# Performance work log

Measured on AMD Instinct MI355X. Metric: run time of the kernel, lower is better.

Reference implementation:

```python
import jax, jax.numpy as jnp
import numpy as np

N_HEAD, D_MODEL, D_HEAD = 16, 1024, 64
QLEN, BSZ, RLEN = 2048, 2, 2048
SCALE = 1.0 / (D_HEAD ** 0.5)


def setup_inputs() -> dict:
    key = jax.random.key(0)
    ks = jax.random.split(key, 7)
    return {
        "w": jax.random.normal(ks[0], (QLEN, BSZ, D_MODEL), dtype=jnp.float32),
        "r": jax.random.normal(ks[1], (RLEN, D_MODEL), dtype=jnp.float32),
        "qkv_w": jax.random.normal(ks[2], (D_MODEL, 3 * N_HEAD * D_HEAD), dtype=jnp.float32) * 0.02,
        "r_net_w": jax.random.normal(ks[3], (D_MODEL, N_HEAD * D_HEAD), dtype=jnp.float32) * 0.02,
        "o_w": jax.random.normal(ks[4], (N_HEAD * D_HEAD, D_MODEL), dtype=jnp.float32) * 0.02,
        "r_r_bias": jax.random.normal(ks[5], (N_HEAD, D_HEAD), dtype=jnp.float32) * 0.02,
        "r_w_bias": jax.random.normal(ks[6], (N_HEAD, D_HEAD), dtype=jnp.float32) * 0.02,
    }


def _rel_shift(x):
    # x: [qlen, rlen, bsz, n_head]
    q, r, b, n = x.shape
    x = jnp.pad(x, ((0, 0), (1, 0), (0, 0), (0, 0)))
    x = x.reshape(r + 1, q, b, n)[1:]
    return x.reshape(q, r, b, n)


def reference(w, r, qkv_w, r_net_w, o_w, r_r_bias, r_w_bias):
    qlen, bsz, _ = w.shape
    rlen = r.shape[0]
    # qkv projection: [qlen, bsz, 3*H*D]
    w_heads = jnp.einsum('ibm,mh->ibh', w, qkv_w)
    w_head_q, w_head_k, w_head_v = jnp.split(w_heads, 3, axis=-1)
    klen = w_head_k.shape[0]
    w_head_q = w_head_q.reshape(qlen, bsz, N_HEAD, D_HEAD)
    w_head_k = w_head_k.reshape(klen, bsz, N_HEAD, D_HEAD)
    w_head_v = w_head_v.reshape(klen, bsz, N_HEAD, D_HEAD)
    # relative position keys: [rlen, H, D]
    r_head_k = jnp.einsum('jm,mh->jh', r, r_net_w).reshape(rlen, N_HEAD, D_HEAD)

    rw_head_q = w_head_q + r_w_bias  # content bias
    rr_head_q = w_head_q + r_r_bias  # position bias
    AC = jnp.einsum('ibnd,jbnd->ijbn', rw_head_q, w_head_k)
    BD = jnp.einsum('ibnd,jnd->ijbn', rr_head_q, r_head_k)
    BD = _rel_shift(BD)[:, :klen]

    attn_score = (AC + BD) * SCALE
    attn_prob = jax.nn.softmax(attn_score, axis=1)  # over klen axis
    attn_vec = jnp.einsum('ijbn,jbnd->ibnd', attn_prob, w_head_v)
    attn_vec = attn_vec.reshape(qlen, bsz, N_HEAD * D_HEAD)
    attn_out = jnp.einsum('ibh,hm->ibm', attn_vec, o_w)
    return (w + attn_out, attn_prob, AC, BD)
```

## Files before the change

### kernel.cpp

```cpp
#include <hip/hip_runtime.h>
#include <hip/hip_bf16.h>


typedef unsigned short u16;
typedef __attribute__((ext_vector_type(8))) short short8;
typedef __attribute__((ext_vector_type(4))) float f32x4;
typedef __attribute__((ext_vector_type(4))) unsigned short u16x4;

__device__ __forceinline__ u16 f2bf(float x){
  unsigned u = __float_as_uint(x);
  u += 0x7fffu + ((u >> 16) & 1u);
  return (u16)(u >> 16);
}
__device__ __forceinline__ float bf2f(u16 s){
  return __uint_as_float(((unsigned)s) << 16);
}
__device__ __forceinline__ f32x4 mfma16(short8 a, short8 b, f32x4 c){
  return __builtin_amdgcn_mfma_f32_16x16x32_bf16(a, b, c, 0, 0, 0);
}
__device__ __forceinline__ void ntst4(float* p, f32x4 v){
  __builtin_nontemporal_store(v, (f32x4*)p);
}


__global__ __launch_bounds__(256) void k_cast(const float* __restrict__ src, u16* __restrict__ dst, int n4){
  int i = blockIdx.x * 256 + threadIdx.x;
  if (i >= n4) return;
  f32x4 v = *(const f32x4*)(src + (size_t)i * 4);
  u16x4 o;
  #pragma unroll
  for (int q = 0; q < 4; ++q) o[q] = f2bf(v[q]);
  *(u16x4*)(dst + (size_t)i * 4) = o;
}

__global__ __launch_bounds__(256) void k_tc(const float* __restrict__ src, u16* __restrict__ dst, int R, int C){
  __shared__ float ld[32][33];
  int c0 = blockIdx.x * 32, r0 = blockIdx.y * 32;
  int t = threadIdx.x;
  int r = t >> 3, c4 = (t & 7) * 4;
  f32x4 v = *(const f32x4*)(src + (size_t)(r0 + r) * C + c0 + c4);
  #pragma unroll
  for (int q = 0; q < 4; ++q) ld[r][c4 + q] = v[q];
  __syncthreads();
  int c = t >> 3, r4 = (t & 7) * 4;
  u16x4 o;
  #pragma unroll
  for (int q = 0; q < 4; ++q) o[q] = f2bf(ld[r4 + q][c]);
  *(u16x4*)(dst + (size_t)(c0 + c) * R + r0 + r4) = o;
}


template<int MODE>
__global__ __launch_bounds__(512) void k_gemm(const u16* __restrict__ A, const u16* __restrict__ Bt,
        u16* __restrict__ o0, u16* __restrict__ o1, u16* __restrict__ o2,
        const float* __restrict__ wres, float* __restrict__ outf)
{
  __shared__ __align__(16) u16 As[128][40];
  __shared__ __align__(16) u16 Bs[256][40];
  const int t = threadIdx.x;
  const int wave = t >> 6, lane = t & 63;
  const int wr = wave >> 2, wc = wave & 3;
  const int g = lane >> 4, li = lane & 15;
  const int m0 = blockIdx.x * 128, n0 = blockIdx.y * 256;
  f32x4 acc[4][4] = {};
  const int ar = t >> 2, ac8 = (t & 3) * 8;
  for (int kt = 0; kt < 32; ++kt){
    int k0 = kt * 32;
    *(short8*)&As[ar][ac8] = *(const short8*)(A + (size_t)(m0 + ar) * 1024 + k0 + ac8);
    #pragma unroll
    for (int u = 0; u < 2; ++u){
      int id = t + 512 * u; int br = id >> 2, bc8 = (id & 3) * 8;
      *(short8*)&Bs[br][bc8] = *(const short8*)(Bt + (size_t)(n0 + br) * 1024 + k0 + bc8);
    }
    __syncthreads();
    short8 af[4], bfv[4];
    #pragma unroll
    for (int mf = 0; mf < 4; ++mf) af[mf] = *(const short8*)&As[wr * 64 + mf * 16 + li][g * 8];
    #pragma unroll
    for (int nf = 0; nf < 4; ++nf) bfv[nf] = *(const short8*)&Bs[wc * 64 + nf * 16 + li][g * 8];
    #pragma unroll
    for (int mf = 0; mf < 4; ++mf)
      #pragma unroll
      for (int nf = 0; nf < 4; ++nf)
        acc[mf][nf] = mfma16(af[mf], bfv[nf], acc[mf][nf]);
    __syncthreads();
  }
  #pragma unroll
  for (int mf = 0; mf < 4; ++mf)
  #pragma unroll
  for (int nf = 0; nf < 4; ++nf)
  #pragma unroll
  for (int r = 0; r < 4; ++r){
    int gr = m0 + wr * 64 + mf * 16 + g * 4 + r;
    int gc = n0 + wc * 64 + nf * 16 + li;
    float v = acc[mf][nf][r];
    if (MODE == 0){
      int part = gc >> 10, hh = gc & 1023;
      int hn = hh >> 6, d = hh & 63;
      int i = gr >> 1, b = gr & 1;
      u16* dst = (part == 0) ? o0 : ((part == 1) ? o1 : o2);
      dst[((((b << 4) + hn) * 2048 + i) << 6) + d] = f2bf(v);
    } else if (MODE == 1){
      int hn = gc >> 6, d = gc & 63;
      o0[((hn * 2048 + gr) << 6) + d] = f2bf(v);
    } else {
      size_t idx = (size_t)gr * 1024 + gc;
      outf[idx] = wres[idx] + v;
    }
  }
}

__global__ __launch_bounds__(256) void k_bias(const u16* __restrict__ Km, const float* __restrict__ bv,
                                              float* __restrict__ out, int total){
  int idx = blockIdx.x * 256 + threadIdx.x;
  if (idx >= total) return;
  int n = (idx >> 11) & 15;
  const u16* kr = Km + ((size_t)idx << 6);
  const float* bp = bv + n * 64;
  float s = 0.f;
  #pragma unroll
  for (int d8 = 0; d8 < 8; ++d8){
    short8 v = *(const short8*)(kr + d8 * 8);
    #pragma unroll
    for (int q = 0; q < 8; ++q) s += bp[d8 * 8 + q] * bf2f((u16)v[q]);
  }
  out[idx] = s;
}

__global__ __launch_bounds__(256) void k_trv(const u16* __restrict__ V, u16* __restrict__ Vt){
  __shared__ __align__(16) u16 ld[64][72];
  int bn = blockIdx.x, j0 = blockIdx.y * 64;
  int t = threadIdx.x;
  #pragma unroll
  for (int u = 0; u < 2; ++u){
    int id = t + 256 * u; int r = id >> 3, c8 = (id & 7) * 8;
    *(short8*)&ld[r][c8] = *(const short8*)(V + ((size_t)(bn * 2048 + j0 + r) << 6) + c8);
  }
  __syncthreads();
  #pragma unroll
  for (int u = 0; u < 2; ++u){
    int id = t + 256 * u; int d = id >> 3, j8 = (id & 7) * 8;
    short8 o;
    #pragma unroll
    for (int q = 0; q < 8; ++q) o[q] = ld[j8 + q][d];
    *(short8*)(Vt + ((size_t)(bn * 64 + d) << 11) + j0 + j8) = o;
  }
}

__global__ __launch_bounds__(512, 4) void k_statsR(const u16* __restrict__ Q, const u16* __restrict__ RK,
        const u16* __restrict__ Kc, const float* __restrict__ bias_ac, const float* __restrict__ bias_bd,
        float* __restrict__ ACo, float* __restrict__ BDo,
        float* __restrict__ m_part, float* __restrict__ l_part)
{
  __shared__ u16 sBD[2][16 * 544];
  __shared__ u16 sB[32 * 271];
  const int t = threadIdx.x, wave = t >> 6, lane = t & 63;
  const int g = lane >> 4, li = lane & 15;
  const int i0 = blockIdx.x * 16, b = blockIdx.y;
  const int jbase = blockIdx.z * 512;
  short8 qa[2][2], qb[2][2];
  #pragma unroll
  for (int nn = 0; nn < 2; ++nn){
    int bn = b * 16 + wave * 2 + nn;
    const u16* qp = Q + ((size_t)(bn * 2048 + i0 + li) << 6) + g * 8;
    qa[nn][0] = *(const short8*)qp;
    qa[nn][1] = *(const short8*)(qp + 32);
    int rowB = i0 + 1 + li; if (rowB > 2047) rowB = 2047;
    const u16* qp2 = Q + ((size_t)(bn * 2048 + rowB) << 6) + g * 8;
    qb[nn][0] = *(const short8*)qp2;
    qb[nn][1] = *(const short8*)(qp2 + 32);
  }
  for (int w2 = t; w2 < 2 * 4352; w2 += 512) ((unsigned*)sBD)[w2] = 0;

  float m_[2][4], l_[2][4];
  #pragma unroll
  for (int nn = 0; nn < 2; ++nn)
    #pragma unroll
    for (int r = 0; r < 4; ++r){ m_[nn][r] = -__builtin_inff(); l_[nn][r] = 0.f; }

  int cur = 0;
  for (int ch = 0; ch < 16; ++ch){
    int j0 = jbase + ch * 32;
    int m = j0 - i0;
    __syncthreads();
    u16* bufA = &sBD[cur][0];
    u16* bufB = &sBD[cur ^ 1][0];

    auto do_tile = [&](int c0, bool case2){
      if (c0 < 0 || c0 > 2032) return;
      int off = c0 - m + (case2 ? 2 : -2047);
      #pragma unroll
      for (int nn = 0; nn < 2; ++nn){
        int n = wave * 2 + nn;
        const u16* rp = RK + ((size_t)(n * 2048 + c0 + li) << 6) + g * 8;
        short8 b0 = *(const short8*)rp;
        short8 b1 = *(const short8*)(rp + 32);
        f32x4 acc = {};
        acc = mfma16(case2 ? qb[nn][0] : qa[nn][0], b0, acc);
        acc = mfma16(case2 ? qb[nn][1] : qa[nn][1], b1, acc);
        float bb = bias_bd[n * 2048 + c0 + li];
        #pragma unroll
        for (int r = 0; r < 4; ++r){
          int fr = g * 4 + r;
          int jw = li + fr + off;
          u16 val = f2bf(acc[r] + bb);
          if ((unsigned)jw < 32u)       bufA[fr * 544 + jw * 17 + n] = val;
          else if ((unsigned)jw < 64u)  bufB[fr * 544 + (jw - 32) * 17 + n] = val;
        }
      }
    };
    if (ch == 0){
      do_tile(m + 2032, false);
      do_tile(m - 32, true);
      do_tile(m - 16, true);
    }
    do_tile(m + 2048, false);
    do_tile(m + 2064, false);
    do_tile(m, true);
    do_tile(m + 16, true);
    __syncthreads();

    #pragma unroll
    for (int nn = 0; nn < 2; ++nn){
      int n = wave * 2 + nn, bn = b * 16 + n;
      float sv[2][4];
      #pragma unroll
      for (int cf = 0; cf < 2; ++cf){
        int jc = j0 + cf * 16 + li;
        const u16* kp = Kc + ((size_t)(bn * 2048 + jc) << 6) + g * 8;
        short8 b0 = *(const short8*)kp;
        short8 b1 = *(const short8*)(kp + 32);
        f32x4 acc = {};
        acc = mfma16(qa[nn][0], b0, acc);
        acc = mfma16(qa[nn][1], b1, acc);
        float ba = bias_ac[bn * 2048 + jc];
        #pragma unroll
        for (int r = 0; r < 4; ++r){
          float av = acc[r] + ba;
          sB[(cf * 16 + li) * 271 + n * 17 + g * 4 + r] = f2bf(av);
          float bd = bf2f(bufA[(g * 4 + r) * 544 + (cf * 16 + li) * 17 + n]);
          sv[cf][r] = (av + bd) * 0.125f;
        }
      }
      float cm[4], mn[4], ps[4];
      #pragma unroll
      for (int r = 0; r < 4; ++r) cm[r] = fmaxf(sv[0][r], sv[1][r]);
      #pragma unroll
      for (int off = 1; off < 16; off <<= 1)
        #pragma unroll
        for (int r = 0; r < 4; ++r) cm[r] = fmaxf(cm[r], __shfl_xor(cm[r], off));
      #pragma unroll
      for (int r = 0; r < 4; ++r){
        mn[r] = fmaxf(m_[nn][r], cm[r]);
        ps[r] = __expf(sv[0][r] - mn[r]) + __expf(sv[1][r] - mn[r]);
      }
      #pragma unroll
      for (int off = 1; off < 16; off <<= 1)
        #pragma unroll
        for (int r = 0; r < 4; ++r) ps[r] += __shfl_xor(ps[r], off);
      #pragma unroll
      for (int r = 0; r < 4; ++r){
        l_[nn][r] = l_[nn][r] * __expf(m_[nn][r] - mn[r]) + ps[r];
        m_[nn][r] = mn[r];
      }
    }
    #pragma unroll
    for (int u = 0; u < 4; ++u){
      int flat4 = t + 512 * u;
      int n4 = (flat4 & 3) * 4, jl = (flat4 >> 2) & 31, row = flat4 >> 7;
      f32x4 v;
      #pragma unroll
      for (int q = 0; q < 4; ++q) v[q] = bf2f(bufA[row * 544 + jl * 17 + n4 + q]);
      ntst4(BDo + (((size_t)(i0 + row) * 2048 + j0 + jl) << 5) + b * 16 + n4, v);
    }
    __syncthreads();
    #pragma unroll
    for (int u = 0; u < 4; ++u){
      int flat4 = t + 512 * u;
      int n4 = (flat4 & 3) * 4, jl = (flat4 >> 2) & 31, row = flat4 >> 7;
      f32x4 v;
      #pragma unroll
      for (int q = 0; q < 4; ++q) v[q] = bf2f(sB[jl * 271 + (n4 + q) * 17 + row]);
      ntst4(ACo + (((size_t)(i0 + row) * 2048 + j0 + jl) << 5) + b * 16 + n4, v);
    }
    for (int w2 = t; w2 < 4352; w2 += 512) ((unsigned*)bufA)[w2] = 0;
    cur ^= 1;
  }
  if (li == 0){
    #pragma unroll
    for (int nn = 0; nn < 2; ++nn)
      #pragma unroll
      for (int r = 0; r < 4; ++r){
        int bn = b * 16 + wave * 2 + nn;
        size_t o = ((size_t)(blockIdx.z * 32 + bn)) * 2048 + i0 + g * 4 + r;
        m_part[o] = m_[nn][r];
        l_part[o] = l_[nn][r];
      }
  }
}

__global__ __launch_bounds__(256) void k_comb(const float* __restrict__ mp, const float* __restrict__ lp,
                                              float* __restrict__ mf, float* __restrict__ lf){
  int idx = blockIdx.x * 256 + threadIdx.x;
  float m = -__builtin_inff();
  #pragma unroll
  for (int js = 0; js < 4; ++js) m = fmaxf(m, mp[js * 65536 + idx]);
  float l = 0.f;
  #pragma unroll
  for (int js = 0; js < 4; ++js) l += lp[js * 65536 + idx] * __expf(mp[js * 65536 + idx] - m);
  mf[idx] = m;
  lf[idx] = l;
}

__global__ __launch_bounds__(512, 4) void k_prob_pv(const u16* __restrict__ Q, const u16* __restrict__ Kc,
        const u16* __restrict__ Vt, const float* __restrict__ bias_ac, const float* __restrict__ BD,
        const float* __restrict__ m_f, const float* __restrict__ l_f,
        float* __restrict__ PROB, float* __restrict__ Ovp)
{
  __shared__ __align__(16) u16 sA[16 * 648];
  __shared__ u16 sB[32 * 271];
  const int t = threadIdx.x, wave = t >> 6, lane = t & 63;
  const int g = lane >> 4, li = lane & 15;
  const int i0 = blockIdx.x * 16, b = blockIdx.y;
  const int jbase = blockIdx.z * 512;
  short8 qa[2][2];
  float m_[2][4], rl_[2][4];
  #pragma unroll
  for (int nn = 0; nn < 2; ++nn){
    int bn = b * 16 + wave * 2 + nn;
    const u16* qp = Q + ((size_t)(bn * 2048 + i0 + li) << 6) + g * 8;
    qa[nn][0] = *(const short8*)qp;
    qa[nn][1] = *(const short8*)(qp + 32);
    #pragma unroll
    for (int r = 0; r < 4; ++r){
      m_[nn][r]  = m_f[bn * 2048 + i0 + g * 4 + r];
      rl_[nn][r] = 1.f / l_f[bn * 2048 + i0 + g * 4 + r];
    }
  }
  f32x4 oacc[2][4] = {};

  f32x4 pfv[4];
  #pragma unroll
  for (int u = 0; u < 4; ++u){
    int flat4 = t + 512 * u;
    int n4 = (flat4 & 3) * 4, jl = (flat4 >> 2) & 31, row = flat4 >> 7;
    pfv[u] = *(const f32x4*)(BD + (((size_t)(i0 + row) * 2048 + jbase + jl) << 5) + b * 16 + n4);
  }

  for (int ch = 0; ch < 16; ++ch){
    int j0 = jbase + ch * 32;
    __syncthreads();
    #pragma unroll
    for (int u = 0; u < 4; ++u){
      int flat4 = t + 512 * u;
      int n4 = (flat4 & 3) * 4, jl = (flat4 >> 2) & 31, row = flat4 >> 7;
      u16x4 o;
      #pragma unroll
      for (int q = 0; q < 4; ++q) o[q] = (u16)(__float_as_uint(pfv[u][q]) >> 16);
      *(u16x4*)&sA[row * 648 + jl * 20 + n4] = o;
    }
    if (ch + 1 < 16){
      #pragma unroll
      for (int u = 0; u < 4; ++u){
        int flat4 = t + 512 * u;
        int n4 = (flat4 & 3) * 4, jl = (flat4 >> 2) & 31, row = flat4 >> 7;
        pfv[u] = *(const f32x4*)(BD + (((size_t)(i0 + row) * 2048 + j0 + 32 + jl) << 5) + b * 16 + n4);
      }
    }
    __syncthreads();
    #pragma unroll
    for (int nn = 0; nn < 2; ++nn){
      int n = wave * 2 + nn, bn = b * 16 + n;
      #pragma unroll
      for (int cf = 0; cf < 2; ++cf){
        int jc = j0 + cf * 16 + li;
        const u16* kp = Kc + ((size_t)(bn * 2048 + jc) << 6) + g * 8;
        short8 b0 = *(const short8*)kp;
        short8 b1 = *(const short8*)(kp + 32);
        f32x4 acc = {};
        acc = mfma16(qa[nn][0], b0, acc);
        acc = mfma16(qa[nn][1], b1, acc);
        float ba = bias_ac[bn * 2048 + jc];
        #pragma unroll
        for (int r = 0; r < 4; ++r){
          float bd = bf2f(sA[(g * 4 + r) * 648 + (cf * 16 + li) * 20 + n]);
          float s = (acc[r] + ba + bd) * 0.125f;
          float p = __expf(s - m_[nn][r]) * rl_[nn][r];
          sB[(cf * 16 + li) * 271 + n * 17 + g * 4 + r] = f2bf(p);
        }
      }
    }
    #pragma unroll
    for (int nn = 0; nn < 2; ++nn){
      int n = wave * 2 + nn, bn = b * 16 + n;
      short8 pa;
      #pragma unroll
      for (int tt = 0; tt < 8; ++tt) pa[tt] = (short)sB[(g * 8 + tt) * 271 + n * 17 + li];
      const u16* vb = Vt + ((size_t)(bn * 64) << 11) + j0 + g * 8;
      #pragma unroll
      for (int vf = 0; vf < 4; ++vf){
        short8 bv = *(const short8*)(vb + ((size_t)(vf * 16 + li) << 11));
        oacc[nn][vf] = mfma16(pa, bv, oacc[nn][vf]);
      }
    }
    __syncthreads();
    #pragma unroll
    for (int u = 0; u < 4; ++u){
      int flat4 = t + 512 * u;
      int n4 = (flat4 & 3) * 4, jl = (flat4 >> 2) & 31, row = flat4 >> 7;
      f32x4 v;
      #pragma unroll
      for (int q = 0; q < 4; ++q) v[q] = bf2f(sB[jl * 271 + (n4 + q) * 17 + row]);
      ntst4(PROB + (((size_t)(i0 + row) * 2048 + j0 + jl) << 5) + b * 16 + n4, v);
    }
  }
  float* op = Ovp + (size_t)blockIdx.z * 4194304;
  #pragma unroll
  for (int nn = 0; nn < 2; ++nn){
    int n = wave * 2 + nn;
    #pragma unroll
    for (int vf = 0; vf < 4; ++vf)
      #pragma unroll
      for (int r = 0; r < 4; ++r)
        op[(size_t)((i0 + g * 4 + r) * 2 + b) * 1024 + n * 64 + vf * 16 + li] = oacc[nn][vf][r];
  }
}

__global__ __launch_bounds__(256) void k_ovred(const float* __restrict__ ovp, u16* __restrict__ ov){
  int i = blockIdx.x * 256 + threadIdx.x;
  const f32x4* p = (const f32x4*)ovp;
  f32x4 s = p[i];
  #pragma unroll
  for (int js = 1; js < 4; ++js) s += p[(size_t)js * 1048576 + i];
  u16x4 o;
  #pragma unroll
  for (int q = 0; q < 4; ++q) o[q] = f2bf(s[q]);
  ((u16x4*)ov)[i] = o;
}


extern "C" void kernel_launch(void* const* d_in, const int* in_sizes, int n_in,
                              void* d_out, int out_size, void* d_ws, size_t ws_size,
                              hipStream_t stream)
{
  const float* w      = (const float*)d_in[0];
  const float* r      = (const float*)d_in[1];
  const float* qkv_w  = (const float*)d_in[2];
  const float* rnet_w = (const float*)d_in[3];
  const float* o_w    = (const float*)d_in[4];
  const float* rrb    = (const float*)d_in[5];
  const float* rwb    = (const float*)d_in[6];

  char* ws = (char*)d_ws;
  size_t off = 0;
  auto alloc = [&](size_t bytes) -> void* {
    void* p = ws + off; off += (bytes + 255) & ~(size_t)255; return p;
  };
  u16* Xbf    = (u16*)alloc((size_t)4096 * 1024 * 2);
  u16* Rbf    = (u16*)alloc((size_t)2048 * 1024 * 2);
  u16* Wqkvt  = (u16*)alloc((size_t)3072 * 1024 * 2);
  u16* Wrt    = (u16*)alloc((size_t)1024 * 1024 * 2);
  u16* Wot    = (u16*)alloc((size_t)1024 * 1024 * 2);
  u16* Qs     = (u16*)alloc((size_t)32 * 2048 * 64 * 2);
  u16* Ks     = (u16*)alloc((size_t)32 * 2048 * 64 * 2);
  u16* Vs     = (u16*)alloc((size_t)32 * 2048 * 64 * 2);
  u16* Vts    = (u16*)alloc((size_t)32 * 64 * 2048 * 2);
  u16* RKs    = (u16*)alloc((size_t)16 * 2048 * 64 * 2);
  float* bias_ac = (float*)alloc((size_t)32 * 2048 * 4);
  float* bias_bd = (float*)alloc((size_t)16 * 2048 * 4);
  float* m_part  = (float*)alloc((size_t)4 * 32 * 2048 * 4);
  float* l_part  = (float*)alloc((size_t)4 * 32 * 2048 * 4);
  float* m_fin   = (float*)alloc((size_t)32 * 2048 * 4);
  float* l_fin   = (float*)alloc((size_t)32 * 2048 * 4);
  float* Ovp     = (float*)alloc((size_t)4 * 4096 * 1024 * 4);
  u16* Ov     = (u16*)alloc((size_t)4096 * 1024 * 2);

  float* out0 = (float*)d_out;
  float* PROB = out0 + 4194304;
  float* ACo  = PROB + 134217728;
  float* BDo  = ACo  + 134217728;

  k_cast<<<dim3(4096), dim3(256), 0, stream>>>(w, Xbf, 1048576);
  k_cast<<<dim3(2048), dim3(256), 0, stream>>>(r, Rbf, 524288);
  k_tc<<<dim3(96, 32), dim3(256), 0, stream>>>(qkv_w,  Wqkvt, 1024, 3072);
  k_tc<<<dim3(32, 32), dim3(256), 0, stream>>>(rnet_w, Wrt,   1024, 1024);
  k_tc<<<dim3(32, 32), dim3(256), 0, stream>>>(o_w,    Wot,   1024, 1024);
  k_gemm<0><<<dim3(32, 12), dim3(512), 0, stream>>>(Xbf, Wqkvt, Qs, Ks, Vs, nullptr, nullptr);
  k_gemm<1><<<dim3(16, 4),  dim3(512), 0, stream>>>(Rbf, Wrt,  RKs, nullptr, nullptr, nullptr, nullptr);
  k_bias<<<dim3(256), dim3(256), 0, stream>>>(Ks,  rwb, bias_ac, 65536);
  k_bias<<<dim3(128), dim3(256), 0, stream>>>(RKs, rrb, bias_bd, 32768);
  k_trv<<<dim3(32, 32), dim3(256), 0, stream>>>(Vs, Vts);
  k_statsR<<<dim3(128, 2, 4), dim3(512), 0, stream>>>(Qs, RKs, Ks, bias_ac, bias_bd, ACo, BDo, m_part, l_part);
  k_comb<<<dim3(256), dim3(256), 0, stream>>>(m_part, l_part, m_fin, l_fin);
  k_prob_pv<<<dim3(128, 2, 4), dim3(512), 0, stream>>>(Qs, Ks, Vts, bias_ac, BDo, m_fin, l_fin, PROB, Ovp);
  k_ovred<<<dim3(4096), dim3(256), 0, stream>>>(Ovp, Ov);
  k_gemm<2><<<dim3(32, 4), dim3(512), 0, stream>>>(Ov, Wot, nullptr, nullptr, nullptr, w, out0);
}
```

Measured before the change: 1.218 ms.

## Recompute scores in stats pass and fuse AC/BD/prob writes into one kernel

The stats kernel now computes only the running max and sum and no longer writes AC and BD. A new fused kernel recomputes the BD ring and AC scores, then writes AC, BD and PROB and does the PV product in one pass. This removes the 512 MB fp32 BD read-back that the old prob kernel needed. In exchange the QK and R-K MFMA work is done twice, and the second kernel carries more shared memory and more stores per chunk, which may lower occupancy.

New measurement: 1.335 ms. 1.1x slower.

```diff
diff --git a/kernel.cpp b/kernel.cpp
--- a/kernel.cpp
+++ b/kernel.cpp
@@ -147,13 +147,24 @@
   }
 }
 
-__global__ __launch_bounds__(512, 4) void k_statsR(const u16* __restrict__ Q, const u16* __restrict__ RK,
+template<typename F>
+__device__ __forceinline__ void ring_step(int ch, int m, F&& do_tile){
+  if (ch == 0){
+    do_tile(m + 2032, false);
+    do_tile(m - 32, true);
+    do_tile(m - 16, true);
+  }
+  do_tile(m + 2048, false);
+  do_tile(m + 2064, false);
+  do_tile(m, true);
+  do_tile(m + 16, true);
+}
+
+__global__ __launch_bounds__(512, 4) void k_stats2(const u16* __restrict__ Q, const u16* __restrict__ RK,
         const u16* __restrict__ Kc, const float* __restrict__ bias_ac, const float* __restrict__ bias_bd,
-        float* __restrict__ ACo, float* __restrict__ BDo,
         float* __restrict__ m_part, float* __restrict__ l_part)
 {
   __shared__ u16 sBD[2][16 * 544];
-  __shared__ u16 sB[32 * 271];
   const int t = threadIdx.x, wave = t >> 6, lane = t & 63;
   const int g = lane >> 4, li = lane & 15;
   const int i0 = blockIdx.x * 16, b = blockIdx.y;
@@ -185,7 +196,6 @@
     __syncthreads();
     u16* bufA = &sBD[cur][0];
     u16* bufB = &sBD[cur ^ 1][0];
-
     auto do_tile = [&](int c0, bool case2){
       if (c0 < 0 || c0 > 2032) return;
       int off = c0 - m + (case2 ? 2 : -2047);
@@ -209,21 +219,159 @@
         }
       }
     };
-    if (ch == 0){
-      do_tile(m + 2032, false);
-      do_tile(m - 32, true);
-      do_tile(m - 16, true);
-    }
-    do_tile(m + 2048, false);
-    do_tile(m + 2064, false);
-    do_tile(m, true);
-    do_tile(m + 16, true);
+    ring_step(ch, m, do_tile);
     __syncthreads();
 
     #pragma unroll
     for (int nn = 0; nn < 2; ++nn){
       int n = wave * 2 + nn, bn = b * 16 + n;
       float sv[2][4];
+      #pragma unroll
+      for (int cf = 0; cf < 2; ++cf){
+        int jc = j0 + cf * 16 + li;
+        const u16* kp = Kc + ((size_t)(bn * 2048 + jc) << 6) + g * 8;
+        short8 b0 = *(const short8*)kp;
+        short8 b1 = *(const short8*)(kp + 32);
+        f32x4 acc = {};
+        acc = mfma16(qa[nn][0], b0, acc);
+        acc = mfma16(qa[nn][1], b1, acc);
+        float ba = bias_ac[bn * 2048 + jc];
+        #pragma unroll
+        for (int r = 0; r < 4; ++r){
+          int ci = (g * 4 + r) * 544 + (cf * 16 + li) * 17 + n;
+          float bd = bf2f(bufA[ci]);
+          bufA[ci] = 0;
+          sv[cf][r] = (acc[r] + ba + bd) * 0.125f;
+        }
+      }
+      float cm[4], mn[4], ps[4];
+      #pragma unroll
+      for (int r = 0; r < 4; ++r) cm[r] = fmaxf(sv[0][r], sv[1][r]);
+      #pragma unroll
+      for (int off = 1; off < 16; off <<= 1)
+        #pragma unroll
+        for (int r = 0; r < 4; ++r) cm[r] = fmaxf(cm[r], __shfl_xor(cm[r], off));
+      #pragma unroll
+      for (int r = 0; r < 4; ++r){
+        mn[r] = fmaxf(m_[nn][r], cm[r]);
+        ps[r] = __expf(sv[0][r] - mn[r]) + __expf(sv[1][r] - mn[r]);
+      }
+      #pragma unroll
+      for (int off = 1; off < 16; off <<= 1)
+        #pragma unroll
+        for (int r = 0; r < 4; ++r) ps[r] += __shfl_xor(ps[r], off);
+      #pragma unroll
+      for (int r = 0; r < 4; ++r){
+        l_[nn][r] = l_[nn][r] * __expf(m_[nn][r] - mn[r]) + ps[r];
+        m_[nn][r] = mn[r];
+      }
+    }
+    cur ^= 1;
+  }
+  if (li == 0){
+    #pragma unroll
+    for (int nn = 0; nn < 2; ++nn)
+      #pragma unroll
+      for (int r = 0; r < 4; ++r){
+        int bn = b * 16 + wave * 2 + nn;
+        size_t o = ((size_t)(blockIdx.z * 32 + bn)) * 2048 + i0 + g * 4 + r;
+        m_part[o] = m_[nn][r];
+        l_part[o] = l_[nn][r];
+      }
+  }
+}
+
+__global__ __launch_bounds__(256) void k_comb(const float* __restrict__ mp, const float* __restrict__ lp,
+                                              float* __restrict__ mf, float* __restrict__ lf){
+  int idx = blockIdx.x * 256 + threadIdx.x;
+  float m = -__builtin_inff();
+  #pragma unroll
+  for (int js = 0; js < 4; ++js) m = fmaxf(m, mp[js * 65536 + idx]);
+  float l = 0.f;
+  #pragma unroll
+  for (int js = 0; js < 4; ++js) l += lp[js * 65536 + idx] * __expf(mp[js * 65536 + idx] - m);
+  mf[idx] = m;
+  lf[idx] = l;
+}
+
+__global__ __launch_bounds__(512, 4) void k_mega(const u16* __restrict__ Q, const u16* __restrict__ RK,
+        const u16* __restrict__ Kc, const u16* __restrict__ Vt,
+        const float* __restrict__ bias_ac, const float* __restrict__ bias_bd,
+        const float* __restrict__ m_f, const float* __restrict__ l_f,
+        float* __restrict__ ACo, float* __restrict__ BDo, float* __restrict__ PROB,
+        float* __restrict__ Ovp)
+{
+  __shared__ u16 sBD[2][16 * 544];
+  __shared__ u16 sAC[32 * 271];
+  __shared__ u16 sP [32 * 271];
+  const int t = threadIdx.x, wave = t >> 6, lane = t & 63;
+  const int g = lane >> 4, li = lane & 15;
+  const int i0 = blockIdx.x * 16, b = blockIdx.y;
+  const int jbase = blockIdx.z * 512;
+  short8 qa[2][2];
+  float m_[2][4], rl_[2][4];
+  #pragma unroll
+  for (int nn = 0; nn < 2; ++nn){
+    int bn = b * 16 + wave * 2 + nn;
+    const u16* qp = Q + ((size_t)(bn * 2048 + i0 + li) << 6) + g * 8;
+    qa[nn][0] = *(const short8*)qp;
+    qa[nn][1] = *(const short8*)(qp + 32);
+    #pragma unroll
+    for (int r = 0; r < 4; ++r){
+      m_[nn][r]  = m_f[bn * 2048 + i0 + g * 4 + r];
+      rl_[nn][r] = 1.f / l_f[bn * 2048 + i0 + g * 4 + r];
+    }
+  }
+  for (int w2 = t; w2 < 2 * 4352; w2 += 512) ((unsigned*)sBD)[w2] = 0;
+  f32x4 oacc[2][4] = {};
+
+  int cur = 0;
+  for (int ch = 0; ch < 16; ++ch){
+    int j0 = jbase + ch * 32;
+    int m = j0 - i0;
+    __syncthreads();
+    u16* bufA = &sBD[cur][0];
+    u16* bufB = &sBD[cur ^ 1][0];
+    {
+      short8 qb[2][2];
+      #pragma unroll
+      for (int nn = 0; nn < 2; ++nn){
+        int bn = b * 16 + wave * 2 + nn;
+        int rowB = i0 + 1 + li; if (rowB > 2047) rowB = 2047;
+        const u16* qp2 = Q + ((size_t)(bn * 2048 + rowB) << 6) + g * 8;
+        qb[nn][0] = *(const short8*)qp2;
+        qb[nn][1] = *(const short8*)(qp2 + 32);
+      }
+      auto do_tile = [&](int c0, bool case2){
+        if (c0 < 0 || c0 > 2032) return;
+        int off = c0 - m + (case2 ? 2 : -2047);
+        #pragma unroll
+        for (int nn = 0; nn < 2; ++nn){
+          int n = wave * 2 + nn;
+          const u16* rp = RK + ((size_t)(n * 2048 + c0 + li) << 6) + g * 8;
+          short8 b0 = *(const short8*)rp;
+          short8 b1 = *(const short8*)(rp + 32);
+          f32x4 acc = {};
+          acc = mfma16(case2 ? qb[nn][0] : qa[nn][0], b0, acc);
+          acc = mfma16(case2 ? qb[nn][1] : qa[nn][1], b1, acc);
+          float bb = bias_bd[n * 2048 + c0 + li];
+          #pragma unroll
+          for (int r = 0; r < 4; ++r){
+            int fr = g * 4 + r;
+            int jw = li + fr + off;
+            u16 val = f2bf(acc[r] + bb);
+            if ((unsigned)jw < 32u)       bufA[fr * 544 + jw * 17 + n] = val;
+            else if ((unsigned)jw < 64u)  bufB[fr * 544 + (jw - 32) * 17 + n] = val;
+          }
+        }
+      };
+      ring_step(ch, m, do_tile);
+    }
+    __syncthreads();
+
+    #pragma unroll
+    for (int nn = 0; nn < 2; ++nn){
+      int n = wave * 2 + nn, bn = b * 16 + n;
       #pragma unroll
       for (int cf = 0; cf < 2; ++cf){
         int jc = j0 + cf * 16 + li;
@@ -237,182 +385,55 @@
         #pragma unroll
         for (int r = 0; r < 4; ++r){
           float av = acc[r] + ba;
-          sB[(cf * 16 + li) * 271 + n * 17 + g * 4 + r] = f2bf(av);
+          sAC[(cf * 16 + li) * 271 + n * 17 + g * 4 + r] = f2bf(av);
           float bd = bf2f(bufA[(g * 4 + r) * 544 + (cf * 16 + li) * 17 + n]);
-          sv[cf][r] = (av + bd) * 0.125f;
+          float s = (av + bd) * 0.125f;
+          float p = __expf(s - m_[nn][r]) * rl_[nn][r];
+          sP[(cf * 16 + li) * 271 + n * 17 + g * 4 + r] = f2bf(p);
         }
       }
-      float cm[4], mn[4], ps[4];
-      #pragma unroll
-      for (int r = 0; r < 4; ++r) cm[r] = fmaxf(sv[0][r], sv[1][r]);
-      #pragma unroll
-      for (int off = 1; off < 16; off <<= 1)
-        #pragma unroll
-        for (int r = 0; r < 4; ++r) cm[r] = fmaxf(cm[r], __shfl_xor(cm[r], off));
-      #pragma unroll
-      for (int r = 0; r < 4; ++r){
-        mn[r] = fmaxf(m_[nn][r], cm[r]);
-        ps[r] = __expf(sv[0][r] - mn[r]) + __expf(sv[1][r] - mn[r]);
-      }
-      #pragma unroll
-      for (int off = 1; off < 16; off <<= 1)
-        #pragma unroll
-        for (int r = 0; r < 4; ++r) ps[r] += __shfl_xor(ps[r], off);
-      #pragma unroll
-      for (int r = 0; r < 4; ++r){
-        l_[nn][r] = l_[nn][r] * __expf(m_[nn][r] - mn[r]) + ps[r];
-        m_[nn][r] = mn[r];
+    }
+    __syncthreads();
+
+    #pragma unroll
+    for (int nn = 0; nn < 2; ++nn){
+      int n = wave * 2 + nn, bn = b * 16 + n;
+      short8 pa;
+      #pragma unroll
+      for (int tt = 0; tt < 8; ++tt) pa[tt] = (short)sP[(g * 8 + tt) * 271 + n * 17 + li];
+      const u16* vb = Vt + ((size_t)(bn * 64) << 11) + j0 + g * 8;
+      #pragma unroll
+      for (int vf = 0; vf < 4; ++vf){
+        short8 bv = *(const short8*)(vb + ((size_t)(vf * 16 + li) << 11));
+        oacc[nn][vf] = mfma16(pa, bv, oacc[nn][vf]);
       }
     }
     #pragma unroll
     for (int u = 0; u < 4; ++u){
       int flat4 = t + 512 * u;
       int n4 = (flat4 & 3) * 4, jl = (flat4 >> 2) & 31, row = flat4 >> 7;
+      u16* src = &bufA[row * 544 + jl * 17 + n4];
       f32x4 v;
       #pragma unroll
-      for (int q = 0; q < 4; ++q) v[q] = bf2f(bufA[row * 544 + jl * 17 + n4 + q]);
+      for (int q = 0; q < 4; ++q) v[q] = bf2f(src[q]);
+      *(u16x4*)src = (u16x4){0, 0, 0, 0};
       ntst4(BDo + (((size_t)(i0 + row) * 2048 + j0 + jl) << 5) + b * 16 + n4, v);
     }
-    __syncthreads();
     #pragma unroll
     for (int u = 0; u < 4; ++u){
       int flat4 = t + 512 * u;
       int n4 = (flat4 & 3) * 4, jl = (flat4 >> 2) & 31, row = flat4 >> 7;
-      f32x4 v;
-      #pragma unroll
-      for (int q = 0; q < 4; ++q) v[q] = bf2f(sB[jl * 271 + (n4 + q) * 17 + row]);
-      ntst4(ACo + (((size_t)(i0 + row) * 2048 + j0 + jl) << 5) + b * 16 + n4, v);
-    }
-    for (int w2 = t; w2 < 4352; w2 += 512) ((unsigned*)bufA)[w2] = 0;
+      f32x4 va, vp;
+      #pragma unroll
+      for (int q = 0; q < 4; ++q){
+        va[q] = bf2f(sAC[jl * 271 + (n4 + q) * 17 + row]);
+        vp[q] = bf2f(sP [jl * 271 + (n4 + q) * 17 + row]);
+      }
+      size_t base = (((size_t)(i0 + row) * 2048 + j0 + jl) << 5) + b * 16 + n4;
+      ntst4(ACo  + base, va);
+      ntst4(PROB + base, vp);
+    }
     cur ^= 1;
-  }
-  if (li == 0){
-    #pragma unroll
-    for (int nn = 0; nn < 2; ++nn)
-      #pragma unroll
-      for (int r = 0; r < 4; ++r){
-        int bn = b * 16 + wave * 2 + nn;
-        size_t o = ((size_t)(blockIdx.z * 32 + bn)) * 2048 + i0 + g * 4 + r;
-        m_part[o] = m_[nn][r];
-        l_part[o] = l_[nn][r];
-      }
-  }
-}
-
-__global__ __launch_bounds__(256) void k_comb(const float* __restrict__ mp, const float* __restrict__ lp,
-                                              float* __restrict__ mf, float* __restrict__ lf){
-  int idx = blockIdx.x * 256 + threadIdx.x;
-  float m = -__builtin_inff();
-  #pragma unroll
-  for (int js = 0; js < 4; ++js) m = fmaxf(m, mp[js * 65536 + idx]);
-  float l = 0.f;
-  #pragma unroll
-  for (int js = 0; js < 4; ++js) l += lp[js * 65536 + idx] * __expf(mp[js * 65536 + idx] - m);
-  mf[idx] = m;
-  lf[idx] = l;
-}
-
-__global__ __launch_bounds__(512, 4) void k_prob_pv(const u16* __restrict__ Q, const u16* __restrict__ Kc,
-        const u16* __restrict__ Vt, const float* __restrict__ bias_ac, const float* __restrict__ BD,
-        const float* __restrict__ m_f, const float* __restrict__ l_f,
-        float* __restrict__ PROB, float* __restrict__ Ovp)
-{
-  __shared__ __align__(16) u16 sA[16 * 648];
-  __shared__ u16 sB[32 * 271];
-  const int t = threadIdx.x, wave = t >> 6, lane = t & 63;
-  const int g = lane >> 4, li = lane & 15;
-  const int i0 = blockIdx.x * 16, b = blockIdx.y;
-  const int jbase = blockIdx.z * 512;
-  short8 qa[2][2];
-  float m_[2][4], rl_[2][4];
-  #pragma unroll
-  for (int nn = 0; nn < 2; ++nn){
-    int bn = b * 16 + wave * 2 + nn;
-    const u16* qp = Q + ((size_t)(bn * 2048 + i0 + li) << 6) + g * 8;
-    qa[nn][0] = *(const short8*)qp;
-    qa[nn][1] = *(const short8*)(qp + 32);
-    #pragma unroll
-    for (int r = 0; r < 4; ++r){
-      m_[nn][r]  = m_f[bn * 2048 + i0 + g * 4 + r];
-      rl_[nn][r] = 1.f / l_f[bn * 2048 + i0 + g * 4 + r];
-    }
-  }
-  f32x4 oacc[2][4] = {};
-
-  f32x4 pfv[4];
-  #pragma unroll
-  for (int u = 0; u < 4; ++u){
-    int flat4 = t + 512 * u;
-    int n4 = (flat4 & 3) * 4, jl = (flat4 >> 2) & 31, row = flat4 >> 7;
-    pfv[u] = *(const f32x4*)(BD + (((size_t)(i0 + row) * 2048 + jbase + jl) << 5) + b * 16 + n4);
-  }
-
-  for (int ch = 0; ch < 16; ++ch){
-    int j0 = jbase + ch * 32;
-    __syncthreads();
-    #pragma unroll
-    for (int u = 0; u < 4; ++u){
-      int flat4 = t + 512 * u;
-      int n4 = (flat4 & 3) * 4, jl = (flat4 >> 2) & 31, row = flat4 >> 7;
-      u16x4 o;
-      #pragma unroll
-      for (int q = 0; q < 4; ++q) o[q] = (u16)(__float_as_uint(pfv[u][q]) >> 16);
-      *(u16x4*)&sA[row * 648 + jl * 20 + n4] = o;
-    }
-    if (ch + 1 < 16){
-      #pragma unroll
-      for (int u = 0; u < 4; ++u){
-        int flat4 = t + 512 * u;
-        int n4 = (flat4 & 3) * 4, jl = (flat4 >> 2) & 31, row = flat4 >> 7;
-        pfv[u] = *(const f32x4*)(BD + (((size_t)(i0 + row) * 2048 + j0 + 32 + jl) << 5) + b * 16 + n4);
-      }
-    }
-    __syncthreads();
-    #pragma unroll
-    for (int nn = 0; nn < 2; ++nn){
-      int n = wave * 2 + nn, bn = b * 16 + n;
-      #pragma unroll
-      for (int cf = 0; cf < 2; ++cf){
-        int jc = j0 + cf * 16 + li;
-        const u16* kp = Kc + ((size_t)(bn * 2048 + jc) << 6) + g * 8;
-        short8 b0 = *(const short8*)kp;
-        short8 b1 = *(const short8*)(kp + 32);
-        f32x4 acc = {};
-        acc = mfma16(qa[nn][0], b0, acc);
-        acc = mfma16(qa[nn][1], b1, acc);
-        float ba = bias_ac[bn * 2048 + jc];
-        #pragma unroll
-        for (int r = 0; r < 4; ++r){
-          float bd = bf2f(sA[(g * 4 + r) * 648 + (cf * 16 + li) * 20 + n]);
-          float s = (acc[r] + ba + bd) * 0.125f;
-          float p = __expf(s - m_[nn][r]) * rl_[nn][r];
-          sB[(cf * 16 + li) * 271 + n * 17 + g * 4 + r] = f2bf(p);
-        }
-      }
-    }
-    #pragma unroll
-    for (int nn = 0; nn < 2; ++nn){
-      int n = wave * 2 + nn, bn = b * 16 + n;
-      short8 pa;
-      #pragma unroll
-      for (int tt = 0; tt < 8; ++tt) pa[tt] = (short)sB[(g * 8 + tt) * 271 + n * 17 + li];
-      const u16* vb = Vt + ((size_t)(bn * 64) << 11) + j0 + g * 8;
-      #pragma unroll
-      for (int vf = 0; vf < 4; ++vf){
-        short8 bv = *(const short8*)(vb + ((size_t)(vf * 16 + li) << 11));
-        oacc[nn][vf] = mfma16(pa, bv, oacc[nn][vf]);
-      }
-    }
-    __syncthreads();
-    #pragma unroll
-    for (int u = 0; u < 4; ++u){
-      int flat4 = t + 512 * u;
-      int n4 = (flat4 & 3) * 4, jl = (flat4 >> 2) & 31, row = flat4 >> 7;
-      f32x4 v;
-      #pragma unroll
-      for (int q = 0; q < 4; ++q) v[q] = bf2f(sB[jl * 271 + (n4 + q) * 17 + row]);
-      ntst4(PROB + (((size_t)(i0 + row) * 2048 + j0 + jl) << 5) + b * 16 + n4, v);
-    }
   }
   float* op = Ovp + (size_t)blockIdx.z * 4194304;
   #pragma unroll
@@ -490,9 +511,9 @@
   k_bias<<<dim3(256), dim3(256), 0, stream>>>(Ks,  rwb, bias_ac, 65536);
   k_bias<<<dim3(128), dim3(256), 0, stream>>>(RKs, rrb, bias_bd, 32768);
   k_trv<<<dim3(32, 32), dim3(256), 0, stream>>>(Vs, Vts);
-  k_statsR<<<dim3(128, 2, 4), dim3(512), 0, stream>>>(Qs, RKs, Ks, bias_ac, bias_bd, ACo, BDo, m_part, l_part);
+  k_stats2<<<dim3(128, 2, 4), dim3(512), 0, stream>>>(Qs, RKs, Ks, bias_ac, bias_bd, m_part, l_part);
   k_comb<<<dim3(256), dim3(256), 0, stream>>>(m_part, l_part, m_fin, l_fin);
-  k_prob_pv<<<dim3(128, 2, 4), dim3(512), 0, stream>>>(Qs, Ks, Vts, bias_ac, BDo, m_fin, l_fin, PROB, Ovp);
+  k_mega<<<dim3(128, 2, 4), dim3(512), 0, stream>>>(Qs, RKs, Ks, Vts, bias_ac, bias_bd, m_fin, l_fin, ACo, BDo, PROB, Ovp);
   k_ovred<<<dim3(4096), dim3(256), 0, stream>>>(Ovp, Ov);
   k_gemm<2><<<dim3(32, 4), dim3(512), 0, stream>>>(Ov, Wot, nullptr, nullptr, nullptr, w, out0);
 }
```

## Write AC/BD/prob outputs directly from registers instead of staging through LDS

Applied to the files above, without the earlier changes.

Removes the LDS staging and vectorized nontemporal store loops for the AC, BD and probability outputs, writing each element straight from the MFMA accumulator lanes to global memory. It also drops a barrier and the separate LDS clear pass, and stores AC and prob at full fp32 instead of via bf16. The cost is that each store is a scattered 4-byte write with large lane stride, which may coalesce poorly on these very large output tensors.

After: 2.845 ms. 2.34x slower.

```diff
diff --git a/kernel.cpp b/kernel.cpp
--- a/kernel.cpp
+++ b/kernel.cpp
@@ -147,13 +147,25 @@
   }
 }
 
-__global__ __launch_bounds__(512, 4) void k_statsR(const u16* __restrict__ Q, const u16* __restrict__ RK,
+template<typename F>
+__device__ __forceinline__ void ring_step(int ch, int m, F&& do_tile){
+  if (ch == 0){
+    do_tile(m + 2032, false);
+    do_tile(m - 32, true);
+    do_tile(m - 16, true);
+  }
+  do_tile(m + 2048, false);
+  do_tile(m + 2064, false);
+  do_tile(m, true);
+  do_tile(m + 16, true);
+}
+
+__global__ __launch_bounds__(512, 4) void k_statsD(const u16* __restrict__ Q, const u16* __restrict__ RK,
         const u16* __restrict__ Kc, const float* __restrict__ bias_ac, const float* __restrict__ bias_bd,
         float* __restrict__ ACo, float* __restrict__ BDo,
         float* __restrict__ m_part, float* __restrict__ l_part)
 {
   __shared__ u16 sBD[2][16 * 544];
-  __shared__ u16 sB[32 * 271];
   const int t = threadIdx.x, wave = t >> 6, lane = t & 63;
   const int g = lane >> 4, li = lane & 15;
   const int i0 = blockIdx.x * 16, b = blockIdx.y;
@@ -209,15 +221,7 @@
         }
       }
     };
-    if (ch == 0){
-      do_tile(m + 2032, false);
-      do_tile(m - 32, true);
-      do_tile(m - 16, true);
-    }
-    do_tile(m + 2048, false);
-    do_tile(m + 2064, false);
-    do_tile(m, true);
-    do_tile(m + 16, true);
+    ring_step(ch, m, do_tile);
     __syncthreads();
 
     #pragma unroll
@@ -237,8 +241,12 @@
         #pragma unroll
         for (int r = 0; r < 4; ++r){
           float av = acc[r] + ba;
-          sB[(cf * 16 + li) * 271 + n * 17 + g * 4 + r] = f2bf(av);
-          float bd = bf2f(bufA[(g * 4 + r) * 544 + (cf * 16 + li) * 17 + n]);
+          size_t gaddr = (((size_t)(i0 + g * 4 + r) * 2048 + jc) << 5) + b * 16 + n;
+          ACo[gaddr] = av;
+          int ci = (g * 4 + r) * 544 + (cf * 16 + li) * 17 + n;
+          float bd = bf2f(bufA[ci]);
+          bufA[ci] = 0;
+          BDo[gaddr] = bd;
           sv[cf][r] = (av + bd) * 0.125f;
         }
       }
@@ -264,26 +272,6 @@
         m_[nn][r] = mn[r];
       }
     }
-    #pragma unroll
-    for (int u = 0; u < 4; ++u){
-      int flat4 = t + 512 * u;
-      int n4 = (flat4 & 3) * 4, jl = (flat4 >> 2) & 31, row = flat4 >> 7;
-      f32x4 v;
-      #pragma unroll
-      for (int q = 0; q < 4; ++q) v[q] = bf2f(bufA[row * 544 + jl * 17 + n4 + q]);
-      ntst4(BDo + (((size_t)(i0 + row) * 2048 + j0 + jl) << 5) + b * 16 + n4, v);
-    }
-    __syncthreads();
-    #pragma unroll
-    for (int u = 0; u < 4; ++u){
-      int flat4 = t + 512 * u;
-      int n4 = (flat4 & 3) * 4, jl = (flat4 >> 2) & 31, row = flat4 >> 7;
-      f32x4 v;
-      #pragma unroll
-      for (int q = 0; q < 4; ++q) v[q] = bf2f(sB[jl * 271 + (n4 + q) * 17 + row]);
-      ntst4(ACo + (((size_t)(i0 + row) * 2048 + j0 + jl) << 5) + b * 16 + n4, v);
-    }
-    for (int w2 = t; w2 < 4352; w2 += 512) ((unsigned*)bufA)[w2] = 0;
     cur ^= 1;
   }
   if (li == 0){
@@ -312,7 +300,7 @@
   lf[idx] = l;
 }
 
-__global__ __launch_bounds__(512, 4) void k_prob_pv(const u16* __restrict__ Q, const u16* __restrict__ Kc,
+__global__ __launch_bounds__(512, 4) void k_probD(const u16* __restrict__ Q, const u16* __restrict__ Kc,
         const u16* __restrict__ Vt, const float* __restrict__ bias_ac, const float* __restrict__ BD,
         const float* __restrict__ m_f, const float* __restrict__ l_f,
         float* __restrict__ PROB, float* __restrict__ Ovp)
@@ -386,6 +374,7 @@
           float bd = bf2f(sA[(g * 4 + r) * 648 + (cf * 16 + li) * 20 + n]);
           float s = (acc[r] + ba + bd) * 0.125f;
           float p = __expf(s - m_[nn][r]) * rl_[nn][r];
+          PROB[(((size_t)(i0 + g * 4 + r) * 2048 + jc) << 5) + b * 16 + n] = p;
           sB[(cf * 16 + li) * 271 + n * 17 + g * 4 + r] = f2bf(p);
         }
       }
@@ -402,16 +391,6 @@
         short8 bv = *(const short8*)(vb + ((size_t)(vf * 16 + li) << 11));
         oacc[nn][vf] = mfma16(pa, bv, oacc[nn][vf]);
       }
-    }
-    __syncthreads();
-    #pragma unroll
-    for (int u = 0; u < 4; ++u){
-      int flat4 = t + 512 * u;
-      int n4 = (flat4 & 3) * 4, jl = (flat4 >> 2) & 31, row = flat4 >> 7;
-      f32x4 v;
-      #pragma unroll
-      for (int q = 0; q < 4; ++q) v[q] = bf2f(sB[jl * 271 + (n4 + q) * 17 + row]);
-      ntst4(PROB + (((size_t)(i0 + row) * 2048 + j0 + jl) << 5) + b * 16 + n4, v);
     }
   }
   float* op = Ovp + (size_t)blockIdx.z * 4194304;
@@ -490,9 +469,9 @@
   k_bias<<<dim3(256), dim3(256), 0, stream>>>(Ks,  rwb, bias_ac, 65536);
   k_bias<<<dim3(128), dim3(256), 0, stream>>>(RKs, rrb, bias_bd, 32768);
   k_trv<<<dim3(32, 32), dim3(256), 0, stream>>>(Vs, Vts);
-  k_statsR<<<dim3(128, 2, 4), dim3(512), 0, stream>>>(Qs, RKs, Ks, bias_ac, bias_bd, ACo, BDo, m_part, l_part);
+  k_statsD<<<dim3(128, 2, 4), dim3(512), 0, stream>>>(Qs, RKs, Ks, bias_ac, bias_bd, ACo, BDo, m_part, l_part);
   k_comb<<<dim3(256), dim3(256), 0, stream>>>(m_part, l_part, m_fin, l_fin);
-  k_prob_pv<<<dim3(128, 2, 4), dim3(512), 0, stream>>>(Qs, Ks, Vts, bias_ac, BDo, m_fin, l_fin, PROB, Ovp);
+  k_probD<<<dim3(128, 2, 4), dim3(512), 0, stream>>>(Qs, Ks, Vts, bias_ac, BDo, m_fin, l_fin, PROB, Ovp);
   k_ovred<<<dim3(4096), dim3(256), 0, stream>>>(Ovp, Ov);
   k_gemm<2><<<dim3(32, 4), dim3(512), 0, stream>>>(Ov, Wot, nullptr, nullptr, nullptr, w, out0);
 }
```

## Compute softmax probabilities from stored AC/BD instead of recomputing QK^T

Applied to the files above, without the earlier changes.

The probability kernel no longer recomputes Q·K scores with MFMA and bias. It reads the already-written AC and BD fp32 outputs, adds them, scales, and applies exp with precomputed max and reciprocal-sum stored in an (i, bn) transposed layout. The combine kernel now emits a transposed max and reciprocal l so they can be loaded as vectors. PROB is written in fp32 straight from registers, removing a shared-memory round trip and a barrier. In exchange the kernel reads twice as much fp32 score data from HBM (AC plus BD, about 1 GB total) instead of only BD, so a compute-bound phase becomes a heavier memory-bound one.

Measured after the change: 1.274 ms. 4.6% more time.

```diff
diff --git a/kernel.cpp b/kernel.cpp
--- a/kernel.cpp
+++ b/kernel.cpp
@@ -147,6 +147,19 @@
   }
 }
 
+template<typename F>
+__device__ __forceinline__ void ring_step(int ch, int m, F&& do_tile){
+  if (ch == 0){
+    do_tile(m + 2032, false);
+    do_tile(m - 32, true);
+    do_tile(m - 16, true);
+  }
+  do_tile(m + 2048, false);
+  do_tile(m + 2064, false);
+  do_tile(m, true);
+  do_tile(m + 16, true);
+}
+
 __global__ __launch_bounds__(512, 4) void k_statsR(const u16* __restrict__ Q, const u16* __restrict__ RK,
         const u16* __restrict__ Kc, const float* __restrict__ bias_ac, const float* __restrict__ bias_bd,
         float* __restrict__ ACo, float* __restrict__ BDo,
@@ -209,15 +222,7 @@
         }
       }
     };
-    if (ch == 0){
-      do_tile(m + 2032, false);
-      do_tile(m - 32, true);
-      do_tile(m - 16, true);
-    }
-    do_tile(m + 2048, false);
-    do_tile(m + 2064, false);
-    do_tile(m, true);
-    do_tile(m + 16, true);
+    ring_step(ch, m, do_tile);
     __syncthreads();
 
     #pragma unroll
@@ -299,52 +304,46 @@
   }
 }
 
-__global__ __launch_bounds__(256) void k_comb(const float* __restrict__ mp, const float* __restrict__ lp,
-                                              float* __restrict__ mf, float* __restrict__ lf){
+__global__ __launch_bounds__(256) void k_comb2(const float* __restrict__ mp, const float* __restrict__ lp,
+                                               float* __restrict__ m_t, float* __restrict__ rl_t){
   int idx = blockIdx.x * 256 + threadIdx.x;
+  int bn = idx & 31, i = idx >> 5;
   float m = -__builtin_inff();
   #pragma unroll
-  for (int js = 0; js < 4; ++js) m = fmaxf(m, mp[js * 65536 + idx]);
+  for (int js = 0; js < 4; ++js) m = fmaxf(m, mp[(size_t)(js * 32 + bn) * 2048 + i]);
   float l = 0.f;
   #pragma unroll
-  for (int js = 0; js < 4; ++js) l += lp[js * 65536 + idx] * __expf(mp[js * 65536 + idx] - m);
-  mf[idx] = m;
-  lf[idx] = l;
-}
-
-__global__ __launch_bounds__(512, 4) void k_prob_pv(const u16* __restrict__ Q, const u16* __restrict__ Kc,
-        const u16* __restrict__ Vt, const float* __restrict__ bias_ac, const float* __restrict__ BD,
-        const float* __restrict__ m_f, const float* __restrict__ l_f,
+  for (int js = 0; js < 4; ++js) l += lp[(size_t)(js * 32 + bn) * 2048 + i] * __expf(mp[(size_t)(js * 32 + bn) * 2048 + i] - m);
+  m_t[idx]  = m;
+  rl_t[idx] = 1.f / l;
+}
+
+__global__ __launch_bounds__(512, 4) void k_probS(const float* __restrict__ AC, const float* __restrict__ BD,
+        const u16* __restrict__ Vt, const float* __restrict__ m_t, const float* __restrict__ rl_t,
         float* __restrict__ PROB, float* __restrict__ Ovp)
 {
-  __shared__ __align__(16) u16 sA[16 * 648];
   __shared__ u16 sB[32 * 271];
   const int t = threadIdx.x, wave = t >> 6, lane = t & 63;
   const int g = lane >> 4, li = lane & 15;
   const int i0 = blockIdx.x * 16, b = blockIdx.y;
   const int jbase = blockIdx.z * 512;
-  short8 qa[2][2];
-  float m_[2][4], rl_[2][4];
-  #pragma unroll
-  for (int nn = 0; nn < 2; ++nn){
-    int bn = b * 16 + wave * 2 + nn;
-    const u16* qp = Q + ((size_t)(bn * 2048 + i0 + li) << 6) + g * 8;
-    qa[nn][0] = *(const short8*)qp;
-    qa[nn][1] = *(const short8*)(qp + 32);
-    #pragma unroll
-    for (int r = 0; r < 4; ++r){
-      m_[nn][r]  = m_f[bn * 2048 + i0 + g * 4 + r];
-      rl_[nn][r] = 1.f / l_f[bn * 2048 + i0 + g * 4 + r];
-    }
-  }
+  const int n4 = (t & 3) * 4, jl = (t >> 2) & 31, r0 = t >> 7;
   f32x4 oacc[2][4] = {};
 
-  f32x4 pfv[4];
+  f32x4 mq[4], rq[4];
   #pragma unroll
   for (int u = 0; u < 4; ++u){
-    int flat4 = t + 512 * u;
-    int n4 = (flat4 & 3) * 4, jl = (flat4 >> 2) & 31, row = flat4 >> 7;
-    pfv[u] = *(const f32x4*)(BD + (((size_t)(i0 + row) * 2048 + jbase + jl) << 5) + b * 16 + n4);
+    int row = r0 + u * 4;
+    mq[u] = *(const f32x4*)(m_t  + (i0 + row) * 32 + b * 16 + n4);
+    rq[u] = *(const f32x4*)(rl_t + (i0 + row) * 32 + b * 16 + n4);
+  }
+
+  f32x4 pfa[4], pfb[4];
+  #pragma unroll
+  for (int u = 0; u < 4; ++u){
+    size_t ad = (((size_t)(i0 + r0 + u * 4) * 2048 + jbase + jl) << 5) + b * 16 + n4;
+    pfa[u] = *(const f32x4*)(AC + ad);
+    pfb[u] = *(const f32x4*)(BD + ad);
   }
 
   for (int ch = 0; ch < 16; ++ch){
@@ -352,44 +351,25 @@
     __syncthreads();
     #pragma unroll
     for (int u = 0; u < 4; ++u){
-      int flat4 = t + 512 * u;
-      int n4 = (flat4 & 3) * 4, jl = (flat4 >> 2) & 31, row = flat4 >> 7;
-      u16x4 o;
-      #pragma unroll
-      for (int q = 0; q < 4; ++q) o[q] = (u16)(__float_as_uint(pfv[u][q]) >> 16);
-      *(u16x4*)&sA[row * 648 + jl * 20 + n4] = o;
+      int row = r0 + u * 4;
+      f32x4 p;
+      #pragma unroll
+      for (int q = 0; q < 4; ++q){
+        float s = (pfa[u][q] + pfb[u][q]) * 0.125f;
+        p[q] = __expf(s - mq[u][q]) * rq[u][q];
+        sB[jl * 271 + (n4 + q) * 17 + row] = f2bf(p[q]);
+      }
+      ntst4(PROB + (((size_t)(i0 + row) * 2048 + j0 + jl) << 5) + b * 16 + n4, p);
     }
     if (ch + 1 < 16){
       #pragma unroll
       for (int u = 0; u < 4; ++u){
-        int flat4 = t + 512 * u;
-        int n4 = (flat4 & 3) * 4, jl = (flat4 >> 2) & 31, row = flat4 >> 7;
-        pfv[u] = *(const f32x4*)(BD + (((size_t)(i0 + row) * 2048 + j0 + 32 + jl) << 5) + b * 16 + n4);
-      }
-    }
-    __syncthreads();
-    #pragma unroll
-    for (int nn = 0; nn < 2; ++nn){
-      int n = wave * 2 + nn, bn = b * 16 + n;
-      #pragma unroll
-      for (int cf = 0; cf < 2; ++cf){
-        int jc = j0 + cf * 16 + li;
-        const u16* kp = Kc + ((size_t)(bn * 2048 + jc) << 6) + g * 8;
-        short8 b0 = *(const short8*)kp;
-        short8 b1 = *(const short8*)(kp + 32);
-        f32x4 acc = {};
-        acc = mfma16(qa[nn][0], b0, acc);
-        acc = mfma16(qa[nn][1], b1, acc);
-        float ba = bias_ac[bn * 2048 + jc];
-        #pragma unroll
-        for (int r = 0; r < 4; ++r){
-          float bd = bf2f(sA[(g * 4 + r) * 648 + (cf * 16 + li) * 20 + n]);
-          float s = (acc[r] + ba + bd) * 0.125f;
-          float p = __expf(s - m_[nn][r]) * rl_[nn][r];
-          sB[(cf * 16 + li) * 271 + n * 17 + g * 4 + r] = f2bf(p);
-        }
-      }
-    }
+        size_t ad = (((size_t)(i0 + r0 + u * 4) * 2048 + j0 + 32 + jl) << 5) + b * 16 + n4;
+        pfa[u] = *(const f32x4*)(AC + ad);
+        pfb[u] = *(const f32x4*)(BD + ad);
+      }
+    }
+    __syncthreads();
     #pragma unroll
     for (int nn = 0; nn < 2; ++nn){
       int n = wave * 2 + nn, bn = b * 16 + n;
@@ -402,16 +382,6 @@
         short8 bv = *(const short8*)(vb + ((size_t)(vf * 16 + li) << 11));
         oacc[nn][vf] = mfma16(pa, bv, oacc[nn][vf]);
       }
-    }
-    __syncthreads();
-    #pragma unroll
-    for (int u = 0; u < 4; ++u){
-      int flat4 = t + 512 * u;
-      int n4 = (flat4 & 3) * 4, jl = (flat4 >> 2) & 31, row = flat4 >> 7;
-      f32x4 v;
-      #pragma unroll
-      for (int q = 0; q < 4; ++q) v[q] = bf2f(sB[jl * 271 + (n4 + q) * 17 + row]);
-      ntst4(PROB + (((size_t)(i0 + row) * 2048 + j0 + jl) << 5) + b * 16 + n4, v);
     }
   }
   float* op = Ovp + (size_t)blockIdx.z * 4194304;
@@ -470,8 +440,8 @@
   float* bias_bd = (float*)alloc((size_t)16 * 2048 * 4);
   float* m_part  = (float*)alloc((size_t)4 * 32 * 2048 * 4);
   float* l_part  = (float*)alloc((size_t)4 * 32 * 2048 * 4);
-  float* m_fin   = (float*)alloc((size_t)32 * 2048 * 4);
-  float* l_fin   = (float*)alloc((size_t)32 * 2048 * 4);
+  float* m_t     = (float*)alloc((size_t)2048 * 32 * 4);
+  float* rl_t    = (float*)alloc((size_t)2048 * 32 * 4);
   float* Ovp     = (float*)alloc((size_t)4 * 4096 * 1024 * 4);
   u16* Ov     = (u16*)alloc((size_t)4096 * 1024 * 2);
 
@@ -491,8 +461,8 @@
   k_bias<<<dim3(128), dim3(256), 0, stream>>>(RKs, rrb, bias_bd, 32768);
   k_trv<<<dim3(32, 32), dim3(256), 0, stream>>>(Vs, Vts);
   k_statsR<<<dim3(128, 2, 4), dim3(512), 0, stream>>>(Qs, RKs, Ks, bias_ac, bias_bd, ACo, BDo, m_part, l_part);
-  k_comb<<<dim3(256), dim3(256), 0, stream>>>(m_part, l_part, m_fin, l_fin);
-  k_prob_pv<<<dim3(128, 2, 4), dim3(512), 0, stream>>>(Qs, Ks, Vts, bias_ac, BDo, m_fin, l_fin, PROB, Ovp);
+  k_comb2<<<dim3(256), dim3(256), 0, stream>>>(m_part, l_part, m_t, rl_t);
+  k_probS<<<dim3(128, 2, 4), dim3(512), 0, stream>>>(ACo, BDo, Vts, m_t, rl_t, PROB, Ovp);
   k_ovred<<<dim3(4096), dim3(256), 0, stream>>>(Ovp, Ov);
   k_gemm<2><<<dim3(32, 4), dim3(512), 0, stream>>>(Ov, Wot, nullptr, nullptr, nullptr, w, out0);
 }
```
